# Optimization experiments

Measured on AMD Instinct MI355X. Metric: run time of the kernel, lower is better.

Reference implementation:

```python
import jax, jax.numpy as jnp
import numpy as np

NSTATES = 16
NCOM = 4
NHIDDEN = 256
BATCH = 262144


def _orthogonal(key, out_dim, in_dim):
    # mimic torch.nn.init.orthogonal_
    big, small = max(out_dim, in_dim), min(out_dim, in_dim)
    a = jax.random.normal(key, (big, small), dtype=jnp.float32)
    q, r = jnp.linalg.qr(a)
    q = q * jnp.sign(jnp.diagonal(r))  # make deterministic / uniform
    if out_dim < in_dim:
        q = q.T
    return q


def setup_inputs() -> dict:
    key = jax.random.key(0)
    k0, k1, k2, k3, k4 = jax.random.split(key, 5)
    zstates = jax.random.normal(k0, (BATCH, NSTATES), dtype=jnp.float32)
    W1 = _orthogonal(k1, NHIDDEN, NSTATES)            # lin1.weight [nhidden, nstates]
    W2 = _orthogonal(k2, NHIDDEN, NHIDDEN)            # lin2.weight
    W3 = _orthogonal(k3, NHIDDEN, NHIDDEN)            # lin3.weight
    W4 = _orthogonal(k4, NSTATES + NCOM, NHIDDEN)     # lin4.weight [nstates+ncom, nhidden]
    return {"zstates": zstates, "W1": W1, "W2": W2, "W3": W3, "W4": W4}


def _mlp(x, W1, W2, W3, W4):
    # torch Linear (no bias): y = x @ W.T
    h = jax.nn.log_sigmoid(x @ W1.T)
    h = h + jax.nn.log_sigmoid(h @ W2.T)
    h = h + jax.nn.log_sigmoid(h @ W3.T)
    return h @ W4.T


def reference(zstates, W1, W2, W3, W4):
    nstates = NSTATES

    def _get_com_dstates(s):  # s: [nstates]
        nnout = _mlp(s, W1, W2, W3, W4)
        dstates = nnout[:nstates]
        com = nnout[nstates:]
        return com, (dstates, com)

    jac_fcn = jax.vmap(jax.jacrev(_get_com_dstates, argnums=0, has_aux=True))
    dcom_jac, (dstates, com) = jac_fcn(zstates)   # dcom_jac: [B, ncom, nstates]
    # [B, nstates, ncom] concat dstates column -> [B, nstates, ncom+1]
    dcom_jac_t = jnp.swapaxes(dcom_jac, -2, -1)
    mat = jnp.concatenate([dcom_jac_t, dstates[..., None]], axis=-1)
    q, r = jnp.linalg.qr(mat)                     # reduced QR: q [B, nstates, ncom+1]
    dstates_ortho = q[..., -1] * r[..., -1, -1:]  # [B, nstates]
    return dstates_ortho
```

## Files before the change

kernel.cpp:

```cpp
#include <hip/hip_runtime.h>
#include <math.h>

#define NS 16
#define NC 4
#define NH 256
#define BATCH 262144
#define EPB 64
#define HSTR 264

typedef _Float16 half8 __attribute__((ext_vector_type(8)));
typedef _Float16 half4v __attribute__((ext_vector_type(4)));
typedef _Float16 half2v __attribute__((ext_vector_type(2)));
typedef float f32x4 __attribute__((ext_vector_type(4)));

#define MFMA16(a, b, c) __builtin_amdgcn_mfma_f32_16x16x32_f16((a), (b), (c), 0, 0, 0)

#define OFF_W2HI   0
#define OFF_W2LO   65536
#define OFF_W3HI   131072
#define OFF_W3LO   196608
#define OFF_W2THI  262144
#define OFF_W2TLO  327680
#define OFF_W3THI  393216
#define OFF_W3TLO  458752
#define OFF_W1PHI  524288
#define OFF_W1PLO  532480
#define OFF_W1THI  540672
#define OFF_W1TLO  544768
#define OFF_W4HI   548864
#define OFF_W4LO   552960
#define WS_HALVES  557056

__device__ __forceinline__ float logsigf(float a) {
    return fminf(a, 0.f) - __logf(1.f + __expf(-fabsf(a)));
}
__device__ __forceinline__ float siggf(float a) {
    return 1.f / (1.f + __expf(a));
}
__device__ __forceinline__ void act2(float a, float& ls, float& g) {
    float e  = __expf(-fabsf(a));
    float om = 1.f + e;
    float r  = __builtin_amdgcn_rcpf(om);
    ls = fminf(a, 0.f) - __logf(om);
    g  = (a >= 0.f) ? e * r : r;
}
__device__ __forceinline__ void split2(float x, _Float16& h, _Float16& l) {
    h = (_Float16)x;
    l = (_Float16)(x - (float)h);
}
__device__ __forceinline__ float wsum16(float v) {
    v += __shfl_xor(v, 1, 64);
    v += __shfl_xor(v, 2, 64);
    v += __shfl_xor(v, 4, 64);
    v += __shfl_xor(v, 8, 64);
    return v;
}
__device__ __forceinline__ unsigned h2u(half2v h) {
    union { half2v h; unsigned u; } c; c.h = h; return c.u;
}
__device__ __forceinline__ half2v u2h(unsigned u) {
    union { half2v h; unsigned u; } c; c.u = u; return c.h;
}
__device__ __forceinline__ half2v pkrtz(float a, float b) {
    auto t = __builtin_amdgcn_cvt_pkrtz(a, b);
    union { decltype(t) s; half2v d; } c; c.s = t; return c.d;
}
__device__ __forceinline__ uint2 packg2(float g0, float g1, float g2, float g3) {
    return make_uint2(h2u(pkrtz(g0, g1)), h2u(pkrtz(g2, g3)));
}
union H4u { half4v v4; half2v v2[2]; };

extern "C" __global__ void __launch_bounds__(256)
prep_big(const float* __restrict__ W2, const float* __restrict__ W3,
         _Float16* __restrict__ ws) {
    const int mat = blockIdx.y;
    const float* W = mat ? W3 : W2;
    _Float16* Whi  = ws + (mat ? OFF_W3HI  : OFF_W2HI);
    _Float16* Wlo  = Whi + 65536;
    _Float16* WThi = ws + (mat ? OFF_W3THI : OFF_W2THI);
    _Float16* WTlo = WThi + 65536;
    const int r = blockIdx.x, c = threadIdx.x;
    float x = W[r * NH + c];
    _Float16 h, l; split2(x, h, l);
    Whi[r * NH + c] = h;  Wlo[r * NH + c] = l;
    WThi[c * NH + r] = h; WTlo[c * NH + r] = l;
}

extern "C" __global__ void __launch_bounds__(256)
prep_small(const float* __restrict__ W1, const float* __restrict__ W4,
           _Float16* __restrict__ ws) {
    _Float16* W1phi = ws + OFF_W1PHI;
    _Float16* W1plo = ws + OFF_W1PLO;
    _Float16* W1Thi = ws + OFF_W1THI;
    _Float16* W1Tlo = ws + OFF_W1TLO;
    _Float16* W4hi  = ws + OFF_W4HI;
    _Float16* W4lo  = ws + OFF_W4LO;
    const int t = threadIdx.x;
    #pragma unroll
    for (int s = 0; s < NS; s++) {
        float x = W1[t * NS + s];
        _Float16 h, l; split2(x, h, l);
        W1phi[t * 32 + s] = h;        W1plo[t * 32 + s] = l;
        W1phi[t * 32 + 16 + s] = (_Float16)0.f;
        W1plo[t * 32 + 16 + s] = (_Float16)0.f;
        W1Thi[s * NH + t] = h;        W1Tlo[s * NH + t] = l;
    }
    #pragma unroll
    for (int q = 0; q < 16; q++) {
        int idx = q * 256 + t;
        float x = W4[idx];
        _Float16 h, l; split2(x, h, l);
        W4hi[idx] = h; W4lo[idx] = l;
    }
}


__device__ __forceinline__ void gemm_fwd1(const _Float16* __restrict__ Ahi,
                                          const _Float16* U,
                                          int w, int lo16, int hi4, f32x4 acc[2][4]) {
    #pragma unroll
    for (int ks = 0; ks < 8; ks++) {
        half8 bh[4];
        #pragma unroll
        for (int n = 0; n < 4; n++)
            bh[n] = *(const half8*)&U[(16 * n + lo16) * HSTR + ks * 32 + hi4 * 8];
        #pragma unroll
        for (int m = 0; m < 2; m++) {
            int woff = (32 * w + 16 * m + lo16) * NH + ks * 32 + hi4 * 8;
            half8 ah = *(const half8*)&Ahi[woff];
            #pragma unroll
            for (int n = 0; n < 4; n++)
                acc[m][n] = MFMA16(ah, bh[n], acc[m][n]);
        }
    }
}

__device__ __forceinline__ void gemm_bwd1(const _Float16* __restrict__ Ahi,
                                          const _Float16* U,
                                          int w, int lo16, int hi4, f32x4 acc[2][8]) {
    #pragma unroll
    for (int ks = 0; ks < 8; ks++) {
        half8 bh[8];
        #pragma unroll
        for (int n = 0; n < 8; n++)
            bh[n] = *(const half8*)&U[(16 * n + lo16) * HSTR + ks * 32 + hi4 * 8];
        #pragma unroll
        for (int m = 0; m < 2; m++) {
            int woff = (32 * w + 16 * m + lo16) * NH + ks * 32 + hi4 * 8;
            half8 ah = *(const half8*)&Ahi[woff];
            #pragma unroll
            for (int n = 0; n < 8; n++)
                acc[m][n] = MFMA16(ah, bh[n], acc[m][n]);
        }
    }
}

__global__ void __launch_bounds__(512, 1)
comet_mfma(const float* __restrict__ Z,
           const float* __restrict__ W4,
           const _Float16* __restrict__ ws,
           float* __restrict__ OUT)
{
    const _Float16* W2hi  = ws + OFF_W2HI;
    const _Float16* W3hi  = ws + OFF_W3HI;
    const _Float16* W2Thi = ws + OFF_W2THI;
    const _Float16* W3Thi = ws + OFF_W3THI;
    const _Float16* W1phi = ws + OFF_W1PHI;
    const _Float16* W1plo = ws + OFF_W1PLO;
    const _Float16* W1Thi = ws + OFF_W1THI;
    const _Float16* W4hi  = ws + OFF_W4HI;
    const _Float16* W4lo  = ws + OFF_W4LO;

    __shared__ __align__(16) _Float16 U[128 * HSTR];
    __shared__ __align__(16) float Jfin[16 * 260];
    __shared__ __align__(16) float Pb[8 * 272];

    const int tid  = threadIdx.x;
    const int l    = tid & 63, w = tid >> 6;
    const int lo16 = l & 15, hi4 = l >> 4;
    const int ebase = blockIdx.x * EPB;
    const int c4 = lo16 & 3;

    float4 vreg[2];
    half2v vregh[2][2];
    #pragma unroll
    for (int m = 0; m < 2; m++) {
        vreg[m] = *(const float4*)&W4[(NS + c4) * NH + 32 * w + 16 * m + 4 * hi4];
        vregh[m][0] = pkrtz(vreg[m].x, vreg[m].y);
        vregh[m][1] = pkrtz(vreg[m].z, vreg[m].w);
    }

    uint2 g1u[2][4], g2u[2][4], g3u[2][4];

    {
        f32x4 acc[2][4];
        #pragma unroll
        for (int m = 0; m < 2; m++)
            #pragma unroll
            for (int n = 0; n < 4; n++) acc[m][n] = (f32x4)(0.f);
        half8 bh[4], bl[4];
        #pragma unroll
        for (int n = 0; n < 4; n++) {
            if (hi4 < 2) {
                const float* zp = &Z[(size_t)(ebase + 16 * n + lo16) * NS + hi4 * 8];
                float4 z0 = *(const float4*)zp;
                float4 z1 = *(const float4*)(zp + 4);
                float zz[8] = {z0.x, z0.y, z0.z, z0.w, z1.x, z1.y, z1.z, z1.w};
                #pragma unroll
                for (int r = 0; r < 8; r++) {
                    _Float16 h, lo; split2(zz[r], h, lo);
                    bh[n][r] = h; bl[n][r] = lo;
                }
            } else {
                #pragma unroll
                for (int r = 0; r < 8; r++) { bh[n][r] = (_Float16)0.f; bl[n][r] = (_Float16)0.f; }
            }
        }
        #pragma unroll
        for (int m = 0; m < 2; m++) {
            int woff = (32 * w + 16 * m + lo16) * 32 + hi4 * 8;
            half8 ah = *(const half8*)&W1phi[woff];
            half8 al = *(const half8*)&W1plo[woff];
            #pragma unroll
            for (int n = 0; n < 4; n++) {
                acc[m][n] = MFMA16(ah, bh[n], acc[m][n]);
                acc[m][n] = MFMA16(al, bh[n], acc[m][n]);
                acc[m][n] = MFMA16(ah, bl[n], acc[m][n]);
            }
        }
        #pragma unroll
        for (int m = 0; m < 2; m++)
            #pragma unroll
            for (int n = 0; n < 4; n++) {
                int hoff = (16 * n + lo16) * HSTR + 32 * w + 16 * m + 4 * hi4;
                float gv[4];
                half4v nh;
                #pragma unroll
                for (int r = 0; r < 4; r++) {
                    float ls, g;
                    act2(acc[m][n][r], ls, g);
                    gv[r] = g;
                    nh[r] = (_Float16)ls;
                }
                g1u[m][n] = packg2(gv[0], gv[1], gv[2], gv[3]);
                *(half4v*)&U[hoff] = nh;
            }
    }
    __syncthreads();

    #pragma unroll
    for (int L = 0; L < 2; L++) {
        f32x4 acc[2][4];
        #pragma unroll
        for (int m = 0; m < 2; m++)
            #pragma unroll
            for (int n = 0; n < 4; n++) acc[m][n] = (f32x4)(0.f);
        gemm_fwd1(L ? W3hi : W2hi, U, w, lo16, hi4, acc);
        __syncthreads();
        #pragma unroll
        for (int m = 0; m < 2; m++)
            #pragma unroll
            for (int n = 0; n < 4; n++) {
                int hoff = (16 * n + lo16) * HSTR + 32 * w + 16 * m + 4 * hi4;
                half4v oh = *(const half4v*)&U[hoff];
                float gv[4];
                half4v nh;
                #pragma unroll
                for (int r = 0; r < 4; r++) {
                    float ls, g;
                    act2(acc[m][n][r], ls, g);
                    gv[r] = g;
                    nh[r] = (_Float16)((float)oh[r] + ls);
                }
                if (L) g3u[m][n] = packg2(gv[0], gv[1], gv[2], gv[3]);
                else   g2u[m][n] = packg2(gv[0], gv[1], gv[2], gv[3]);
                *(half4v*)&U[hoff] = nh;
            }
        __syncthreads();
    }

    {
        const int et = w & 3, kh = w >> 2;
        f32x4 acc = (f32x4)(0.f);
        #pragma unroll
        for (int i = 0; i < 4; i++) {
            int ks = 4 * kh + i;
            int boff = (16 * et + lo16) * HSTR + ks * 32 + hi4 * 8;
            half8 bh = *(const half8*)&U[boff];
            int woff = lo16 * NH + ks * 32 + hi4 * 8;
            half8 ah = *(const half8*)&W4hi[woff];
            half8 al = *(const half8*)&W4lo[woff];
            acc = MFMA16(ah, bh, acc);
            acc = MFMA16(al, bh, acc);
        }
        #pragma unroll
        for (int r = 0; r < 4; r++)
            Pb[w * 272 + (hi4 * 4 + r) * 17 + lo16] = acc[r];
    }
    __syncthreads();

    #pragma unroll
    for (int p = 0; p < 2; p++) {
        #pragma unroll
        for (int m = 0; m < 2; m++)
            #pragma unroll
            for (int n = 0; n < 8; n++) {
                const int src = (l & 48) | (4 * (n & 3) + (lo16 >> 2));
                const int et = 2 * p + (n >> 2);
                const int kbase = 32 * w + 16 * m + 4 * hi4;
                half2v g01 = u2h((unsigned)__shfl((int)g3u[m][et].x, src, 64));
                half2v g23 = u2h((unsigned)__shfl((int)g3u[m][et].y, src, 64));
                H4u t;
                t.v2[0] = vregh[m][0] * g01;
                t.v2[1] = vregh[m][1] * g23;
                *(half4v*)&U[(16 * n + lo16) * HSTR + kbase] = t.v4;
            }
        __syncthreads();

        f32x4 acc2[2][8];
        #pragma unroll
        for (int m = 0; m < 2; m++)
            #pragma unroll
            for (int n = 0; n < 8; n++) acc2[m][n] = (f32x4)(0.f);
        gemm_bwd1(W3Thi, U, w, lo16, hi4, acc2);
        __syncthreads();

        #pragma unroll
        for (int m = 0; m < 2; m++)
            #pragma unroll
            for (int n = 0; n < 8; n++) {
                const int src = (l & 48) | (4 * (n & 3) + (lo16 >> 2));
                const int et = 2 * p + (n >> 2);
                const int kbase = 32 * w + 16 * m + 4 * hi4;
                half2v g01 = u2h((unsigned)__shfl((int)g2u[m][et].x, src, 64));
                half2v g23 = u2h((unsigned)__shfl((int)g2u[m][et].y, src, 64));
                float gg[4];
                #pragma unroll
                for (int r = 0; r < 4; r++) {
                    gg[r] = vreg[m][r] + acc2[m][n][r];
                    acc2[m][n][r] = gg[r];
                }
                H4u t;
                t.v2[0] = pkrtz(gg[0], gg[1]) * g01;
                t.v2[1] = pkrtz(gg[2], gg[3]) * g23;
                *(half4v*)&U[(16 * n + lo16) * HSTR + kbase] = t.v4;
            }
        __syncthreads();

        gemm_bwd1(W2Thi, U, w, lo16, hi4, acc2);
        __syncthreads();

        #pragma unroll
        for (int m = 0; m < 2; m++)
            #pragma unroll
            for (int n = 0; n < 8; n++) {
                const int src = (l & 48) | (4 * (n & 3) + (lo16 >> 2));
                const int et = 2 * p + (n >> 2);
                const int kbase = 32 * w + 16 * m + 4 * hi4;
                half2v g01 = u2h((unsigned)__shfl((int)g1u[m][et].x, src, 64));
                half2v g23 = u2h((unsigned)__shfl((int)g1u[m][et].y, src, 64));
                H4u t;
                t.v2[0] = pkrtz(acc2[m][n][0], acc2[m][n][1]) * g01;
                t.v2[1] = pkrtz(acc2[m][n][2], acc2[m][n][3]) * g23;
                *(half4v*)&U[(16 * n + lo16) * HSTR + kbase] = t.v4;
            }
        __syncthreads();

        {
            f32x4 accj = (f32x4)(0.f);
            #pragma unroll
            for (int ks = 0; ks < 8; ks++) {
                int boff = (16 * w + lo16) * HSTR + ks * 32 + hi4 * 8;
                half8 bh = *(const half8*)&U[boff];
                int woff = lo16 * NH + ks * 32 + hi4 * 8;
                half8 ah = *(const half8*)&W1Thi[woff];
                accj = MFMA16(ah, bh, accj);
            }
            #pragma unroll
            for (int r = 0; r < 4; r++)
                Jfin[(4 * hi4 + r) * 260 + 128 * p + 16 * w + lo16] = accj[r];
        }
        __syncthreads();
    }

    #pragma unroll
    for (int half = 0; half < 2; half++) {
        const int e = 8 * w + 4 * half + hi4, s = lo16;
        float acol[4];
        #pragma unroll
        for (int c = 0; c < 4; c++) acol[c] = Jfin[s * 260 + 4 * e + c];
        const int et = e >> 4, c16 = e & 15;
        float dval = Pb[et * 272 + s * 17 + c16] + Pb[(et + 4) * 272 + s * 17 + c16];
        #pragma unroll
        for (int c = 0; c < 4; c++) {
            float n2 = wsum16(acol[c] * acol[c]);
            float inv = (n2 > 1e-30f) ? (1.0f / sqrtf(n2)) : 0.0f;
            float q = acol[c] * inv;
            #pragma unroll
            for (int cc = c + 1; cc < 4; cc++) {
                float pj = wsum16(acol[cc] * q);
                acol[cc] -= pj * q;
            }
            float pd = wsum16(dval * q);
            dval -= pd * q;
        }
        OUT[(size_t)(ebase + e) * NS + s] = dval;
    }
}

__device__ __forceinline__ float dot4f(float4 a, float4 b) {
    return a.x*b.x + a.y*b.y + a.z*b.z + a.w*b.w;
}

__global__ void __launch_bounds__(256, 2)
comet_fused_f32(const float* __restrict__ Z,
                const float* __restrict__ W1,
                const float* __restrict__ W2,
                const float* __restrict__ W3,
                const float* __restrict__ W4,
                float* __restrict__ OUT)
{
    __shared__ __align__(16) float h_lds[4][4][NH];
    __shared__ __align__(16) float m_lds[4][4][NH][NC];

    const int l = threadIdx.x & 63;
    const int w = threadIdx.x >> 6;
    float (*hb)[NH]     = h_lds[w];
    float (*mb)[NH][NC] = m_lds[w];
    const int ebase = (blockIdx.x * 4 + w) * 4;

    float d1g[4][4], d2g[4][4], d3g[4][4];

    {
        float acc[4][4];
        #pragma unroll
        for (int j = 0; j < 4; j++)
            #pragma unroll
            for (int e = 0; e < 4; e++) acc[j][e] = 0.f;
        #pragma unroll
        for (int s4 = 0; s4 < 4; s4++) {
            float4 wf[4];
            #pragma unroll
            for (int j = 0; j < 4; j++)
                wf[j] = *(const float4*)&W1[(l + 64*j) * NS + s4*4];
            #pragma unroll
            for (int e = 0; e < 4; e++) {
                float4 xv = *(const float4*)&Z[(ebase + e) * NS + s4*4];
                #pragma unroll
                for (int j = 0; j < 4; j++) acc[j][e] += dot4f(wf[j], xv);
            }
        }
        #pragma unroll
        for (int j = 0; j < 4; j++)
            #pragma unroll
            for (int e = 0; e < 4; e++) {
                float a = acc[j][e];
                d1g[j][e] = siggf(a);
                hb[e][l + 64*j] = logsigf(a);
            }
    }
    __syncthreads();

#define FWD_LAYER(WPTR, GARR)                                                   \
    {                                                                           \
        float acc[4][4];                                                        \
        _Pragma("unroll")                                                       \
        for (int j = 0; j < 4; j++) {                                           \
            _Pragma("unroll")                                                   \
            for (int e = 0; e < 4; e++) acc[j][e] = 0.f;                        \
        }                                                                       \
        _Pragma("unroll 2")                                                     \
        for (int kk = 0; kk < NH; kk += 4) {                                    \
            float wv[4][4];                                                     \
            _Pragma("unroll")                                                   \
            for (int j = 0; j < 4; j++) {                                       \
                float4 t = *(const float4*)&WPTR[(l + 64*j) * NH + kk];         \
                wv[0][j] = t.x; wv[1][j] = t.y; wv[2][j] = t.z; wv[3][j] = t.w; \
            }                                                                   \
            _Pragma("unroll")                                                   \
            for (int e = 0; e < 4; e++) {                                       \
                float4 hv = *(const float4*)&hb[e][kk];                         \
                _Pragma("unroll")                                               \
                for (int j = 0; j < 4; j++)                                     \
                    acc[j][e] += wv[0][j]*hv.x + wv[1][j]*hv.y                  \
                               + wv[2][j]*hv.z + wv[3][j]*hv.w;                 \
            }                                                                   \
        }                                                                       \
        __syncthreads();                                                        \
        _Pragma("unroll")                                                       \
        for (int j = 0; j < 4; j++) {                                           \
            _Pragma("unroll")                                                   \
            for (int e = 0; e < 4; e++) {                                       \
                float a = acc[j][e];                                            \
                GARR[j][e] = siggf(a);                                          \
                hb[e][l + 64*j] += logsigf(a);                                  \
            }                                                                   \
        }                                                                       \
        __syncthreads();                                                        \
    }

    FWD_LAYER(W2, d2g)
    FWD_LAYER(W3, d3g)
#undef FWD_LAYER

    const int e4 = l >> 4, s4 = l & 15;
    float dval = 0.f;
    {
        #pragma unroll 2
        for (int kk = 0; kk < NH; kk += 4) {
            float4 wf = *(const float4*)&W4[s4 * NH + kk];
            float4 hv = *(const float4*)&hb[e4][kk];
            dval += dot4f(wf, hv);
        }
    }

    float gacc[4][4][4];
    float vf[4][4];
    #pragma unroll
    for (int c = 0; c < 4; c++)
        #pragma unroll
        for (int j = 0; j < 4; j++)
            vf[c][j] = W4[(NS + c) * NH + l + 64*j];
    #pragma unroll
    for (int e = 0; e < 4; e++)
        #pragma unroll
        for (int c = 0; c < 4; c++)
            #pragma unroll
            for (int j = 0; j < 4; j++)
                gacc[e][c][j] = vf[c][j];
    #pragma unroll
    for (int j = 0; j < 4; j++)
        #pragma unroll
        for (int e = 0; e < 4; e++) {
            float g = d3g[j][e];
            float4 mv = make_float4(vf[0][j]*g, vf[1][j]*g, vf[2][j]*g, vf[3][j]*g);
            *(float4*)&mb[e][l + 64*j][0] = mv;
        }
    __syncthreads();

#define BWD_GEMM(WPTR)                                                          \
    {                                                                           \
        _Pragma("unroll 2")                                                     \
        for (int r = 0; r < NH; r++) {                                          \
            float wc[4];                                                        \
            _Pragma("unroll")                                                   \
            for (int j = 0; j < 4; j++) wc[j] = WPTR[r * NH + l + 64*j];        \
            _Pragma("unroll")                                                   \
            for (int e = 0; e < 4; e++) {                                       \
                float4 mv = *(const float4*)&mb[e][r][0];                       \
                _Pragma("unroll")                                               \
                for (int j = 0; j < 4; j++) {                                   \
                    gacc[e][0][j] += wc[j]*mv.x;                                \
                    gacc[e][1][j] += wc[j]*mv.y;                                \
                    gacc[e][2][j] += wc[j]*mv.z;                                \
                    gacc[e][3][j] += wc[j]*mv.w;                                \
                }                                                               \
            }                                                                   \
        }                                                                       \
    }

    BWD_GEMM(W3)
    __syncthreads();
    #pragma unroll
    for (int j = 0; j < 4; j++)
        #pragma unroll
        for (int e = 0; e < 4; e++) {
            float g = d2g[j][e];
            float4 mv = make_float4(gacc[e][0][j]*g, gacc[e][1][j]*g,
                                    gacc[e][2][j]*g, gacc[e][3][j]*g);
            *(float4*)&mb[e][l + 64*j][0] = mv;
        }
    __syncthreads();
    BWD_GEMM(W2)
#undef BWD_GEMM
    __syncthreads();
    #pragma unroll
    for (int j = 0; j < 4; j++)
        #pragma unroll
        for (int e = 0; e < 4; e++) {
            float g = d1g[j][e];
            float4 mv = make_float4(gacc[e][0][j]*g, gacc[e][1][j]*g,
                                    gacc[e][2][j]*g, gacc[e][3][j]*g);
            *(float4*)&mb[e][l + 64*j][0] = mv;
        }
    __syncthreads();

    const int c4 = l >> 4;
    float jv[4] = {0.f, 0.f, 0.f, 0.f};
    #pragma unroll 4
    for (int r = 0; r < NH; r++) {
        float w1v = W1[r * NS + s4];
        #pragma unroll
        for (int e = 0; e < 4; e++) jv[e] += mb[e][r][c4] * w1v;
    }
    __syncthreads();

    float* jlds = (float*)hb;
    #pragma unroll
    for (int e = 0; e < 4; e++) jlds[e * 64 + c4 * 16 + s4] = jv[e];
    __syncthreads();

    float acol[4];
    acol[0] = jlds[e4 * 64 +      s4];
    acol[1] = jlds[e4 * 64 + 16 + s4];
    acol[2] = jlds[e4 * 64 + 32 + s4];
    acol[3] = jlds[e4 * 64 + 48 + s4];
    #pragma unroll
    for (int c = 0; c < 4; c++) {
        float n2 = wsum16(acol[c] * acol[c]);
        float inv = (n2 > 1e-30f) ? (1.0f / sqrtf(n2)) : 0.0f;
        float q = acol[c] * inv;
        #pragma unroll
        for (int cc = c + 1; cc < 4; cc++) {
            float p = wsum16(acol[cc] * q);
            acol[cc] -= p * q;
        }
        float pd = wsum16(dval * q);
        dval -= pd * q;
    }
    OUT[ebase * NS + l] = dval;
}

extern "C" void kernel_launch(void* const* d_in, const int* in_sizes, int n_in,
                              void* d_out, int out_size, void* d_ws, size_t ws_size,
                              hipStream_t stream) {
    const float* Z  = (const float*)d_in[0];
    const float* W1 = (const float*)d_in[1];
    const float* W2 = (const float*)d_in[2];
    const float* W3 = (const float*)d_in[3];
    const float* W4 = (const float*)d_in[4];
    float* OUT = (float*)d_out;

    const size_t need = (size_t)WS_HALVES * sizeof(_Float16);

    if (ws_size >= need) {
        _Float16* ws = (_Float16*)d_ws;
        hipLaunchKernelGGL(prep_big, dim3(NH, 2), dim3(NH), 0, stream, W2, W3, ws);
        hipLaunchKernelGGL(prep_small, dim3(1), dim3(NH), 0, stream, W1, W4, ws);
        hipLaunchKernelGGL(comet_mfma, dim3(BATCH / EPB), dim3(512), 0, stream,
                           Z, W4, ws, OUT);
    } else {
        hipLaunchKernelGGL(comet_fused_f32, dim3(BATCH / 16), dim3(256), 0, stream,
                           Z, W1, W2, W3, W4, OUT);
    }
}
```

Measured before the change: 796.4 us.

## Reorder backward column layout to drop cross-lane shuffles of gate values

Changes the mapping of (element, com-column) pairs to the 16-row tiles so each lane already holds its own gate values, which removes the __shfl calls in the three backward scaling loops. The W4 com rows are staged in shared memory (fp32 and fp16 copies) and read per tile, instead of being held in registers. The final QR gather uses the matching new Jfin column index. This trades shuffle traffic for extra LDS reads and a little more shared memory.

```diff
diff --git a/kernel.cpp b/kernel.cpp
--- a/kernel.cpp
+++ b/kernel.cpp
@@ -174,20 +174,21 @@
     __shared__ __align__(16) _Float16 U[128 * HSTR];
     __shared__ __align__(16) float Jfin[16 * 260];
     __shared__ __align__(16) float Pb[8 * 272];
+    __shared__ __align__(16) float Vb[4 * 260];
+    __shared__ __align__(16) _Float16 Vbh[4 * 264];
 
     const int tid  = threadIdx.x;
     const int l    = tid & 63, w = tid >> 6;
     const int lo16 = l & 15, hi4 = l >> 4;
     const int ebase = blockIdx.x * EPB;
-    const int c4 = lo16 & 3;
-
-    float4 vreg[2];
-    half2v vregh[2][2];
-    #pragma unroll
-    for (int m = 0; m < 2; m++) {
-        vreg[m] = *(const float4*)&W4[(NS + c4) * NH + 32 * w + 16 * m + 4 * hi4];
-        vregh[m][0] = pkrtz(vreg[m].x, vreg[m].y);
-        vregh[m][1] = pkrtz(vreg[m].z, vreg[m].w);
+
+    #pragma unroll
+    for (int i = 0; i < 2; i++) {
+        int idx = i * 512 + tid;
+        int c = idx >> 8, k = idx & 255;
+        float x = W4[(NS + c) * NH + k];
+        Vb[c * 260 + k] = x;
+        Vbh[c * 264 + k] = (_Float16)x;
     }
 
     uint2 g1u[2][4], g2u[2][4], g3u[2][4];
@@ -301,19 +302,23 @@
 
     #pragma unroll
     for (int p = 0; p < 2; p++) {
+        const int kbase = 32 * w + 4 * hi4;
+
         #pragma unroll
         for (int m = 0; m < 2; m++)
             #pragma unroll
             for (int n = 0; n < 8; n++) {
-                const int src = (l & 48) | (4 * (n & 3) + (lo16 >> 2));
-                const int et = 2 * p + (n >> 2);
-                const int kbase = 32 * w + 16 * m + 4 * hi4;
-                half2v g01 = u2h((unsigned)__shfl((int)g3u[m][et].x, src, 64));
-                half2v g23 = u2h((unsigned)__shfl((int)g3u[m][et].y, src, 64));
+                const int c  = n >> 1;
+                const int et = 2 * p + (n & 1);
+                const int kb = kbase + 16 * m;
+                half4v vh4 = *(const half4v*)&Vbh[c * 264 + kb];
+                H4u vv; vv.v4 = vh4;
+                half2v g01 = u2h(g3u[m][et].x);
+                half2v g23 = u2h(g3u[m][et].y);
                 H4u t;
-                t.v2[0] = vregh[m][0] * g01;
-                t.v2[1] = vregh[m][1] * g23;
-                *(half4v*)&U[(16 * n + lo16) * HSTR + kbase] = t.v4;
+                t.v2[0] = vv.v2[0] * g01;
+                t.v2[1] = vv.v2[1] * g23;
+                *(half4v*)&U[(16 * n + lo16) * HSTR + kb] = t.v4;
             }
         __syncthreads();
 
@@ -329,21 +334,22 @@
         for (int m = 0; m < 2; m++)
             #pragma unroll
             for (int n = 0; n < 8; n++) {
-                const int src = (l & 48) | (4 * (n & 3) + (lo16 >> 2));
-                const int et = 2 * p + (n >> 2);
-                const int kbase = 32 * w + 16 * m + 4 * hi4;
-                half2v g01 = u2h((unsigned)__shfl((int)g2u[m][et].x, src, 64));
-                half2v g23 = u2h((unsigned)__shfl((int)g2u[m][et].y, src, 64));
+                const int c  = n >> 1;
+                const int et = 2 * p + (n & 1);
+                const int kb = kbase + 16 * m;
+                f32x4 vf = *(const f32x4*)&Vb[c * 260 + kb];
+                half2v g01 = u2h(g2u[m][et].x);
+                half2v g23 = u2h(g2u[m][et].y);
                 float gg[4];
                 #pragma unroll
                 for (int r = 0; r < 4; r++) {
-                    gg[r] = vreg[m][r] + acc2[m][n][r];
+                    gg[r] = vf[r] + acc2[m][n][r];
                     acc2[m][n][r] = gg[r];
                 }
                 H4u t;
                 t.v2[0] = pkrtz(gg[0], gg[1]) * g01;
                 t.v2[1] = pkrtz(gg[2], gg[3]) * g23;
-                *(half4v*)&U[(16 * n + lo16) * HSTR + kbase] = t.v4;
+                *(half4v*)&U[(16 * n + lo16) * HSTR + kb] = t.v4;
             }
         __syncthreads();
 
@@ -354,15 +360,14 @@
         for (int m = 0; m < 2; m++)
             #pragma unroll
             for (int n = 0; n < 8; n++) {
-                const int src = (l & 48) | (4 * (n & 3) + (lo16 >> 2));
-                const int et = 2 * p + (n >> 2);
-                const int kbase = 32 * w + 16 * m + 4 * hi4;
-                half2v g01 = u2h((unsigned)__shfl((int)g1u[m][et].x, src, 64));
-                half2v g23 = u2h((unsigned)__shfl((int)g1u[m][et].y, src, 64));
+                const int et = 2 * p + (n & 1);
+                const int kb = kbase + 16 * m;
+                half2v g01 = u2h(g1u[m][et].x);
+                half2v g23 = u2h(g1u[m][et].y);
                 H4u t;
                 t.v2[0] = pkrtz(acc2[m][n][0], acc2[m][n][1]) * g01;
                 t.v2[1] = pkrtz(acc2[m][n][2], acc2[m][n][3]) * g23;
-                *(half4v*)&U[(16 * n + lo16) * HSTR + kbase] = t.v4;
+                *(half4v*)&U[(16 * n + lo16) * HSTR + kb] = t.v4;
             }
         __syncthreads();
 
@@ -386,9 +391,10 @@
     #pragma unroll
     for (int half = 0; half < 2; half++) {
         const int e = 8 * w + 4 * half + hi4, s = lo16;
+        const int cb = 128 * (e >> 5) + 16 * ((e >> 4) & 1) + (e & 15);
         float acol[4];
         #pragma unroll
-        for (int c = 0; c < 4; c++) acol[c] = Jfin[s * 260 + 4 * e + c];
+        for (int c = 0; c < 4; c++) acol[c] = Jfin[s * 260 + cb + 32 * c];
         const int et = e >> 4, c16 = e & 15;
         float dval = Pb[et * 272 + s * 17 + c16] + Pb[(et + 4) * 272 + s * 17 + c16];
         #pragma unroll
```

Result: faster. 740.1 us (-7.1%).
